# Optimization experiments

Measured on AMD Instinct MI355X. Metric: run time of the kernel, lower is better.

## Reference

```python
import jax, jax.numpy as jnp
import numpy as np

N_NODES = 50000
N_EDGES = 800000
IN_DIM = 64
HID = 64
NUM_GRAPHS = 512


def _gcn_conv(x, W, b, row, col, norm, n):
    # PyG GCNConv: h = x @ W; out[col] += norm * h[row]; out += b
    h = x @ W  # [N, HID]
    msg = h[row] * norm[:, None]  # [E', HID]
    out = jax.ops.segment_sum(msg, col, num_segments=n)
    return out + b


def setup_inputs() -> dict:
    key = jax.random.key(0)
    ks = jax.random.split(key, 12)
    x = jax.random.normal(ks[0], (N_NODES, IN_DIM), dtype=jnp.float32)
    edge_index = jax.random.randint(ks[1], (2, N_EDGES), 0, N_NODES, dtype=jnp.int64)
    batch = jnp.sort(jax.random.randint(ks[2], (N_NODES,), 0, NUM_GRAPHS, dtype=jnp.int64))
    s = 0.05
    W1 = jax.random.normal(ks[3], (IN_DIM, HID), dtype=jnp.float32) * s
    b1 = jnp.zeros((HID,), dtype=jnp.float32)
    W2 = jax.random.normal(ks[4], (HID, HID), dtype=jnp.float32) * s
    b2 = jnp.zeros((HID,), dtype=jnp.float32)
    W3 = jax.random.normal(ks[5], (HID, HID), dtype=jnp.float32) * s
    b3 = jnp.zeros((HID,), dtype=jnp.float32)
    lin_W = jax.random.normal(ks[6], (HID, 1), dtype=jnp.float32) * s
    lin_b = jnp.zeros((1,), dtype=jnp.float32)
    return {"x": x, "W1": W1, "b1": b1, "W2": W2, "b2": b2, "W3": W3,
            "b3": b3, "lin_W": lin_W, "lin_b": lin_b,
            "edge_index": edge_index, "batch": batch}


def reference(x, W1, b1, W2, b2, W3, b3, lin_W, lin_b, edge_index, batch):
    n = x.shape[0]
    # add self-loops (GCNConv default add_self_loops=True)
    loop = jnp.arange(n, dtype=edge_index.dtype)
    row = jnp.concatenate([edge_index[0], loop])  # source
    col = jnp.concatenate([edge_index[1], loop])  # target (aggregation index)
    # symmetric degree normalization: deg over targets with unit weights
    deg = jax.ops.segment_sum(jnp.ones_like(col, dtype=x.dtype), col, num_segments=n)
    dinv = jnp.where(deg > 0, jax.lax.rsqrt(deg), 0.0)
    norm = dinv[row] * dinv[col]  # [E+N]

    h = jax.nn.relu(_gcn_conv(x, W1, b1, row, col, norm, n))
    h = jax.nn.relu(_gcn_conv(h, W2, b2, row, col, norm, n))
    h = _gcn_conv(h, W3, b3, row, col, norm, n)

    # global_mean_pool over batch ids
    sums = jax.ops.segment_sum(h, batch, num_segments=NUM_GRAPHS)
    cnt = jax.ops.segment_sum(jnp.ones((n,), dtype=h.dtype), batch, num_segments=NUM_GRAPHS)
    pooled = sums / jnp.maximum(cnt, 1.0)[:, None]
    # dropout p=0.5 is identity in eval mode
    return pooled @ lin_W + lin_b  # [NUM_GRAPHS, 1]
```

## Files before the change

### kernel.cpp

```cpp
#include <hip/hip_runtime.h>
#include <hip/hip_fp16.h>

#define NN 50000
#define NE 800000
#define HD 64
#define NG 512
#define NBK 196
#define NBL 196
#define M_CNT (NBK * NBL)
#define NBS 151
#define GEMM_BLOCKS 3125


__global__ __launch_bounds__(256) void bucket_count(const int* __restrict__ col,
                                                    const int* __restrict__ batch,
                                                    int* __restrict__ counts,
                                                    int* __restrict__ beg,
                                                    int* __restrict__ endx,
                                                    float* __restrict__ pooled) {
    __shared__ int hist[256];
    int tid = threadIdx.x, blk = blockIdx.x;
    hist[tid] = 0;
    __syncthreads();
    int base = blk * 4096;
#pragma unroll
    for (int k = 0; k < 16; ++k) {
        int e = base + k * 256 + tid;
        if (e < NE) atomicAdd(&hist[col[e] >> 8], 1);
    }
    int t = blk * 256 + tid;
    if (t < NG * HD) pooled[t] = 0.f;
    if (t < NN) {
        int g = batch[t];
        if (t == 0 || batch[t - 1] != g) beg[g] = t;
        if (t == NN - 1 || batch[t + 1] != g) endx[g] = t + 1;
    }
    __syncthreads();
    if (tid < NBK) counts[tid * NBL + blk] = hist[tid];
}

__global__ __launch_bounds__(256) void block_reduce(const int* __restrict__ src,
                                                    int* __restrict__ bsum) {
    __shared__ int ws[4];
    int tid = threadIdx.x, lane = tid & 63, wid = tid >> 6;
    int i = blockIdx.x * 256 + tid;
    int v = (i < M_CNT) ? src[i] : 0;
#pragma unroll
    for (int off = 32; off > 0; off >>= 1) v += __shfl_down(v, off, 64);
    if (lane == 0) ws[wid] = v;
    __syncthreads();
    if (tid == 0) bsum[blockIdx.x] = ws[0] + ws[1] + ws[2] + ws[3];
}

__global__ __launch_bounds__(256) void block_scan(const int* __restrict__ src,
                                                  const int* __restrict__ bsum,
                                                  int* __restrict__ dst) {
    __shared__ int ws[4];
    __shared__ int spref;
    int tid = threadIdx.x, lane = tid & 63, wid = tid >> 6;
    int i = blockIdx.x * 256 + tid;
    int v = (i < M_CNT) ? src[i] : 0;
    int inc = v;
#pragma unroll
    for (int off = 1; off < 64; off <<= 1) {
        int t = __shfl_up(inc, off, 64);
        if (lane >= off) inc += t;
    }
    if (lane == 63) ws[wid] = inc;
    if (wid == 0) {
        int pref = 0;
        for (int base = 0; base < NBS; base += 64) {
            int k = base + lane;
            int bv = (k < NBS && k < blockIdx.x) ? bsum[k] : 0;
#pragma unroll
            for (int off = 32; off > 0; off >>= 1) bv += __shfl_down(bv, off, 64);
            pref += bv;
        }
        if (lane == 0) spref = pref;
    }
    __syncthreads();
    int woff = 0;
    for (int k = 0; k < wid; ++k) woff += ws[k];
    if (i < M_CNT) dst[i] = spref + woff + inc - v;
}

__global__ __launch_bounds__(256) void gemm1_scatter(const float* __restrict__ x,
                                                     const float* __restrict__ W1,
                                                     __half* __restrict__ h16,
                                                     const int* __restrict__ row,
                                                     const int* __restrict__ col,
                                                     const int* __restrict__ counts_ex,
                                                     unsigned* __restrict__ packed) {
    if (blockIdx.x < GEMM_BLOCKS) {
        __shared__ float Is[16][64];
        int t = threadIdx.x;
        int c = t & 63, r4 = t >> 6;
        float wcol[64];
#pragma unroll
        for (int k = 0; k < 64; ++k) wcol[k] = W1[k * HD + c];
        int row0 = blockIdx.x * 16;
        for (int i = t; i < 16 * 64; i += 256)
            Is[i >> 6][i & 63] = x[(row0 + (i >> 6)) * HD + (i & 63)];
        __syncthreads();
        float a0 = 0.f, a1 = 0.f, a2 = 0.f, a3 = 0.f;
        const float4* i0p = (const float4*)&Is[r4 + 0][0];
        const float4* i1p = (const float4*)&Is[r4 + 4][0];
        const float4* i2p = (const float4*)&Is[r4 + 8][0];
        const float4* i3p = (const float4*)&Is[r4 + 12][0];
#pragma unroll
        for (int q = 0; q < 16; ++q) {
            float4 i0 = i0p[q], i1 = i1p[q], i2 = i2p[q], i3 = i3p[q];
            float w0 = wcol[4 * q + 0], w1 = wcol[4 * q + 1];
            float w2 = wcol[4 * q + 2], w3 = wcol[4 * q + 3];
            a0 += i0.x * w0; a0 += i0.y * w1; a0 += i0.z * w2; a0 += i0.w * w3;
            a1 += i1.x * w0; a1 += i1.y * w1; a1 += i1.z * w2; a1 += i1.w * w3;
            a2 += i2.x * w0; a2 += i2.y * w1; a2 += i2.z * w2; a2 += i2.w * w3;
            a3 += i3.x * w0; a3 += i3.y * w1; a3 += i3.z * w2; a3 += i3.w * w3;
        }
        h16[(row0 + r4 + 0) * HD + c] = __float2half(a0);
        h16[(row0 + r4 + 4) * HD + c] = __float2half(a1);
        h16[(row0 + r4 + 8) * HD + c] = __float2half(a2);
        h16[(row0 + r4 + 12) * HD + c] = __float2half(a3);
    } else {
        __shared__ int cur[256];
        int tid = threadIdx.x, blk = blockIdx.x - GEMM_BLOCKS;
        cur[tid] = 0;
        __syncthreads();
        int base = blk * 4096;
#pragma unroll
        for (int k = 0; k < 16; ++k) {
            int e = base + k * 256 + tid;
            if (e < NE) {
                int c = col[e], r = row[e];
                int b = c >> 8;
                int lpos = atomicAdd(&cur[b], 1);
                int pos = counts_ex[b * NBL + blk] + lpos;
                packed[pos] = (unsigned)r | ((unsigned)(c & 255) << 16);
            }
        }
    }
}

__global__ __launch_bounds__(256) void csr_build(const unsigned* __restrict__ packed,
                                                 const int* __restrict__ counts_ex,
                                                 int* __restrict__ rowptr,
                                                 float* __restrict__ dinv,
                                                 __half* __restrict__ h16,
                                                 int* __restrict__ esrc) {
    __shared__ int hist[256];
    __shared__ int ws[4];
    __shared__ int lrp[256];
    __shared__ float sdinv[256];
    int bkt = blockIdx.x, tid = threadIdx.x;
    int s = counts_ex[bkt * NBL];
    int e = (bkt == NBK - 1) ? NE : counts_ex[(bkt + 1) * NBL];
    hist[tid] = 0;
    __syncthreads();
    for (int j = s + tid; j < e; j += 256)
        atomicAdd(&hist[(packed[j] >> 16) & 255], 1);
    __syncthreads();
    int lane = tid & 63, wid = tid >> 6;
    int v = hist[tid], inc = v;
#pragma unroll
    for (int off = 1; off < 64; off <<= 1) {
        int t = __shfl_up(inc, off, 64);
        if (lane >= off) inc += t;
    }
    if (lane == 63) ws[wid] = inc;
    __syncthreads();
    int woff = 0;
    for (int k = 0; k < wid; ++k) woff += ws[k];
    int excl = s + woff + inc - v;
    int node = bkt * 256 + tid;
    float dv = rsqrtf((float)(v + 1));
    if (node < NN) {
        rowptr[node] = excl;
        dinv[node] = dv;
    }
    if (bkt == 0 && tid == 0) rowptr[NN] = NE;
    lrp[tid] = excl;
    sdinv[tid] = dv;
    hist[tid] = 0;
    __syncthreads();
    {
        int nrows = (bkt == NBK - 1) ? (NN - 195 * 256) : 256;
        __half2* hb16 = (__half2*)(h16 + (size_t)bkt * 256 * HD);
        for (int i = tid; i < nrows * 32; i += 256) {
            float d = sdinv[i >> 5];
            float2 f = __half22float2(hb16[i]);
            hb16[i] = __floats2half2_rn(d * f.x, d * f.y);
        }
    }
    for (int j = s + tid; j < e; j += 256) {
        unsigned p = packed[j];
        int lc = (p >> 16) & 255;
        int slot = lrp[lc] + atomicAdd(&hist[lc], 1);
        esrc[slot] = (int)(p & 0xFFFF);
    }
}

template <bool POOL>
__global__ __launch_bounds__(256) void gather_fx(const __half* __restrict__ hp,
                                                 const int* __restrict__ rowptr,
                                                 const int* __restrict__ esrc,
                                                 const float* __restrict__ dinv,
                                                 const float* __restrict__ b,
                                                 const float* __restrict__ Wnext,
                                                 __half* __restrict__ hnext,
                                                 const int* __restrict__ batch,
                                                 float* __restrict__ pooled) {
    __shared__ float rowbuf[4][64];
    int tid = threadIdx.x, lane = tid & 63, wid = tid >> 6;
    int p = lane >> 5, c = lane & 31;
    int node = __builtin_amdgcn_readfirstlane(blockIdx.x * 4 + wid);
    const __half2* hv = (const __half2*)hp;

    float di = dinv[node];
    float2 self = __half22float2(hv[node * 32 + c]);
    float2 bb = ((const float2*)b)[c];

    float wcol[POOL ? 1 : 64];
    if (!POOL) {
#pragma unroll
        for (int k = 0; k < 64; ++k) wcol[k] = Wnext[k * HD + lane];
    }

    int s = rowptr[node], e = rowptr[node + 1];
    float2 acc = {0.f, 0.f};
    int j = s;
    for (; j + 8 <= e; j += 8) {
        int t0 = esrc[j + 0], t1 = esrc[j + 1], t2 = esrc[j + 2], t3 = esrc[j + 3];
        int t4 = esrc[j + 4], t5 = esrc[j + 5], t6 = esrc[j + 6], t7 = esrc[j + 7];
        int a0 = p ? t1 : t0;
        int a1 = p ? t3 : t2;
        int a2 = p ? t5 : t4;
        int a3 = p ? t7 : t6;
        float2 f0 = __half22float2(hv[a0 * 32 + c]);
        float2 f1 = __half22float2(hv[a1 * 32 + c]);
        float2 f2 = __half22float2(hv[a2 * 32 + c]);
        float2 f3 = __half22float2(hv[a3 * 32 + c]);
        acc.x += (f0.x + f1.x) + (f2.x + f3.x);
        acc.y += (f0.y + f1.y) + (f2.y + f3.y);
    }
    if (j < e) {
        int t0 = esrc[j + 0] & 0xFFFF, t1 = esrc[j + 1] & 0xFFFF;
        int t2 = esrc[j + 2] & 0xFFFF, t3 = esrc[j + 3] & 0xFFFF;
        int t4 = esrc[j + 4] & 0xFFFF, t5 = esrc[j + 5] & 0xFFFF;
        int t6 = esrc[j + 6] & 0xFFFF, t7 = esrc[j + 7] & 0xFFFF;
        int i0 = j + p, i1 = j + 2 + p, i2 = j + 4 + p, i3 = j + 6 + p;
        int a0 = p ? t1 : t0;
        int a1 = p ? t3 : t2;
        int a2 = p ? t5 : t4;
        int a3 = p ? t7 : t6;
        a0 = (i0 < e) ? a0 : t0;
        a1 = (i1 < e) ? a1 : t0;
        a2 = (i2 < e) ? a2 : t0;
        a3 = (i3 < e) ? a3 : t0;
        float m0 = (i0 < e) ? 1.f : 0.f;
        float m1 = (i1 < e) ? 1.f : 0.f;
        float m2 = (i2 < e) ? 1.f : 0.f;
        float m3 = (i3 < e) ? 1.f : 0.f;
        float2 f0 = __half22float2(hv[a0 * 32 + c]);
        float2 f1 = __half22float2(hv[a1 * 32 + c]);
        float2 f2 = __half22float2(hv[a2 * 32 + c]);
        float2 f3 = __half22float2(hv[a3 * 32 + c]);
        acc.x += m0 * f0.x + m1 * f1.x + m2 * f2.x + m3 * f3.x;
        acc.y += m0 * f0.y + m1 * f1.y + m2 * f2.y + m3 * f3.y;
    }
    acc.x += __shfl_xor(acc.x, 32, 64);
    acc.y += __shfl_xor(acc.y, 32, 64);

    if (POOL) {
        if (p == 0) {
            float vx = di * (acc.x + self.x) + bb.x;
            float vy = di * (acc.y + self.y) + bb.y;
            int g = batch[node];
            atomicAdd(&pooled[g * HD + 2 * c], vx);
            atomicAdd(&pooled[g * HD + 2 * c + 1], vy);
        }
    } else {
        if (p == 0) {
            rowbuf[wid][2 * c]     = fmaxf(di * (acc.x + self.x) + bb.x, 0.f);
            rowbuf[wid][2 * c + 1] = fmaxf(di * (acc.y + self.y) + bb.y, 0.f);
        }
        float outc = 0.f;
        const float4* rb4 = (const float4*)&rowbuf[wid][0];
#pragma unroll
        for (int jj = 0; jj < 16; ++jj) {
            float4 r = rb4[jj];
            outc += r.x * wcol[4 * jj + 0] + r.y * wcol[4 * jj + 1]
                  + r.z * wcol[4 * jj + 2] + r.w * wcol[4 * jj + 3];
        }
        hnext[(size_t)node * HD + lane] = __float2half(di * outc);
    }
}

__global__ __launch_bounds__(64) void final_kernel(const float* __restrict__ pooled,
                                                   const int* __restrict__ beg,
                                                   const int* __restrict__ endx,
                                                   const float* __restrict__ lin_W,
                                                   const float* __restrict__ lin_b,
                                                   float* __restrict__ out) {
    int g = blockIdx.x, d = threadIdx.x;
    float cnt = (float)(endx[g] - beg[g]);
    float v = pooled[g * HD + d] / fmaxf(cnt, 1.f) * lin_W[d];
#pragma unroll
    for (int off = 32; off > 0; off >>= 1) v += __shfl_down(v, off, 64);
    if (d == 0) out[g] = v + lin_b[0];
}

extern "C" void kernel_launch(void* const* d_in, const int* in_sizes, int n_in,
                              void* d_out, int out_size, void* d_ws, size_t ws_size,
                              hipStream_t stream) {
    const float* x     = (const float*)d_in[0];
    const float* W1    = (const float*)d_in[1];
    const float* b1    = (const float*)d_in[2];
    const float* W2    = (const float*)d_in[3];
    const float* b2    = (const float*)d_in[4];
    const float* W3    = (const float*)d_in[5];
    const float* b3    = (const float*)d_in[6];
    const float* lin_W = (const float*)d_in[7];
    const float* lin_b = (const float*)d_in[8];
    const int* edge_index = (const int*)d_in[9];
    const int* batch      = (const int*)d_in[10];
    const int* row = edge_index;
    const int* col = edge_index + NE;
    float* out = (float*)d_out;

    __half*   h16a      = (__half*)d_ws;
    __half*   h16b      = h16a + (size_t)NN * HD;
    int*      esrc      = (int*)(h16b + (size_t)NN * HD);
    unsigned* packed    = (unsigned*)(esrc + NE + 64);
    int*      counts    = (int*)(packed + NE);
    int*      counts_ex = counts + M_CNT;
    int*      rowptr    = counts_ex + M_CNT;
    float*    dinv      = (float*)(rowptr + NN + 2);
    int*      bsum      = (int*)(dinv + NN);
    float*    pooled    = (float*)(bsum + 256);
    int*      beg       = (int*)(pooled + NG * HD);
    int*      endx      = beg + NG;

    bucket_count<<<NBL, 256, 0, stream>>>(col, batch, counts, beg, endx, pooled);
    block_reduce<<<NBS, 256, 0, stream>>>(counts, bsum);
    block_scan<<<NBS, 256, 0, stream>>>(counts, bsum, counts_ex);
    gemm1_scatter<<<GEMM_BLOCKS + NBL, 256, 0, stream>>>(x, W1, h16a, row, col,
                                                         counts_ex, packed);
    csr_build<<<NBK, 256, 0, stream>>>(packed, counts_ex, rowptr, dinv,
                                       h16a, esrc);

    const int GB = NN / 4;

    gather_fx<false><<<GB, 256, 0, stream>>>(h16a, rowptr, esrc, dinv, b1, W2,
                                             h16b, batch, pooled);
    gather_fx<false><<<GB, 256, 0, stream>>>(h16b, rowptr, esrc, dinv, b2, W3,
                                             h16a, batch, pooled);
    gather_fx<true><<<GB, 256, 0, stream>>>(h16a, rowptr, esrc, dinv, b3, nullptr,
                                            nullptr, batch, pooled);

    final_kernel<<<NG, 64, 0, stream>>>(pooled, beg, endx, lin_W, lin_b, out);
}
```

Before: 255.3 us.

## Replace two-level bucket CSR build with per-node atomic counting and scatter

Drops the bucketed counting sort (bucket counts, reduce and scan, packed scatter, per-bucket CSR build) in favour of per-node global atomic degree counts, a single scan over nodes that also writes dinv, and a direct atomic-cursor scatter of source ids into esrc. The dinv scaling moves into the first GEMM epilogue, so there is no separate pass that rescales h16. Launch count falls from five kernels to a memset plus three. In exchange, each edge now does a global atomic on a random node counter, both at count time and at fill time. Edge order within a row also becomes nondeterministic, which changes the fp16 summation order.

Result: slower. 296.7 us (+16.2%).

```diff
diff --git a/kernel.cpp b/kernel.cpp
--- a/kernel.cpp
+++ b/kernel.cpp
@@ -7,26 +7,29 @@
 #define NG 512
 #define NBK 196
 #define NBL 196
-#define M_CNT (NBK * NBL)
-#define NBS 151
 #define GEMM_BLOCKS 3125
 
 
-__global__ __launch_bounds__(256) void bucket_count(const int* __restrict__ col,
-                                                    const int* __restrict__ batch,
-                                                    int* __restrict__ counts,
-                                                    int* __restrict__ beg,
-                                                    int* __restrict__ endx,
-                                                    float* __restrict__ pooled) {
-    __shared__ int hist[256];
+__global__ __launch_bounds__(256) void hist(const int* __restrict__ col,
+                                            const int* __restrict__ batch,
+                                            int* __restrict__ cnt,
+                                            int* __restrict__ bsum,
+                                            int* __restrict__ beg,
+                                            int* __restrict__ endx,
+                                            float* __restrict__ pooled) {
+    __shared__ int histL[256];
     int tid = threadIdx.x, blk = blockIdx.x;
-    hist[tid] = 0;
+    histL[tid] = 0;
     __syncthreads();
     int base = blk * 4096;
 #pragma unroll
     for (int k = 0; k < 16; ++k) {
         int e = base + k * 256 + tid;
-        if (e < NE) atomicAdd(&hist[col[e] >> 8], 1);
+        if (e < NE) {
+            int c = col[e];
+            atomicAdd(&cnt[c], 1);
+            atomicAdd(&histL[c >> 8], 1);
+        }
     }
     int t = blk * 256 + tid;
     if (t < NG * HD) pooled[t] = 0.f;
@@ -36,30 +39,19 @@
         if (t == NN - 1 || batch[t + 1] != g) endx[g] = t + 1;
     }
     __syncthreads();
-    if (tid < NBK) counts[tid * NBL + blk] = hist[tid];
-}
-
-__global__ __launch_bounds__(256) void block_reduce(const int* __restrict__ src,
-                                                    int* __restrict__ bsum) {
-    __shared__ int ws[4];
-    int tid = threadIdx.x, lane = tid & 63, wid = tid >> 6;
-    int i = blockIdx.x * 256 + tid;
-    int v = (i < M_CNT) ? src[i] : 0;
-#pragma unroll
-    for (int off = 32; off > 0; off >>= 1) v += __shfl_down(v, off, 64);
-    if (lane == 0) ws[wid] = v;
-    __syncthreads();
-    if (tid == 0) bsum[blockIdx.x] = ws[0] + ws[1] + ws[2] + ws[3];
-}
-
-__global__ __launch_bounds__(256) void block_scan(const int* __restrict__ src,
-                                                  const int* __restrict__ bsum,
-                                                  int* __restrict__ dst) {
+    if (tid < NBK) atomicAdd(&bsum[tid], histL[tid]);
+}
+
+__global__ __launch_bounds__(256) void nscan(const int* __restrict__ cnt,
+                                             const int* __restrict__ bsum,
+                                             int* __restrict__ rowptr,
+                                             int* __restrict__ cursor,
+                                             float* __restrict__ dinv) {
     __shared__ int ws[4];
     __shared__ int spref;
     int tid = threadIdx.x, lane = tid & 63, wid = tid >> 6;
     int i = blockIdx.x * 256 + tid;
-    int v = (i < M_CNT) ? src[i] : 0;
+    int v = (i < NN) ? cnt[i] : 0;
     int inc = v;
 #pragma unroll
     for (int off = 1; off < 64; off <<= 1) {
@@ -69,9 +61,9 @@
     if (lane == 63) ws[wid] = inc;
     if (wid == 0) {
         int pref = 0;
-        for (int base = 0; base < NBS; base += 64) {
+        for (int base = 0; base < NBK; base += 64) {
             int k = base + lane;
-            int bv = (k < NBS && k < blockIdx.x) ? bsum[k] : 0;
+            int bv = (k < NBK && k < blockIdx.x) ? bsum[k] : 0;
 #pragma unroll
             for (int off = 32; off > 0; off >>= 1) bv += __shfl_down(bv, off, 64);
             pref += bv;
@@ -81,16 +73,23 @@
     __syncthreads();
     int woff = 0;
     for (int k = 0; k < wid; ++k) woff += ws[k];
-    if (i < M_CNT) dst[i] = spref + woff + inc - v;
-}
-
-__global__ __launch_bounds__(256) void gemm1_scatter(const float* __restrict__ x,
-                                                     const float* __restrict__ W1,
-                                                     __half* __restrict__ h16,
-                                                     const int* __restrict__ row,
-                                                     const int* __restrict__ col,
-                                                     const int* __restrict__ counts_ex,
-                                                     unsigned* __restrict__ packed) {
+    if (i < NN) {
+        int excl = spref + woff + inc - v;
+        rowptr[i] = excl;
+        cursor[i] = excl;
+        dinv[i] = rsqrtf((float)(v + 1));
+    }
+    if (i == 0) rowptr[NN] = NE;
+}
+
+__global__ __launch_bounds__(256) void gemm1_fill(const float* __restrict__ x,
+                                                  const float* __restrict__ W1,
+                                                  const float* __restrict__ dinv,
+                                                  __half* __restrict__ h16,
+                                                  const int* __restrict__ row,
+                                                  const int* __restrict__ col,
+                                                  int* __restrict__ cursor,
+                                                  int* __restrict__ esrc) {
     if (blockIdx.x < GEMM_BLOCKS) {
         __shared__ float Is[16][64];
         int t = threadIdx.x;
@@ -99,6 +98,10 @@
 #pragma unroll
         for (int k = 0; k < 64; ++k) wcol[k] = W1[k * HD + c];
         int row0 = blockIdx.x * 16;
+        float d0 = dinv[row0 + r4 + 0];
+        float d1 = dinv[row0 + r4 + 4];
+        float d2 = dinv[row0 + r4 + 8];
+        float d3 = dinv[row0 + r4 + 12];
         for (int i = t; i < 16 * 64; i += 256)
             Is[i >> 6][i & 63] = x[(row0 + (i >> 6)) * HD + (i & 63)];
         __syncthreads();
@@ -117,85 +120,22 @@
             a2 += i2.x * w0; a2 += i2.y * w1; a2 += i2.z * w2; a2 += i2.w * w3;
             a3 += i3.x * w0; a3 += i3.y * w1; a3 += i3.z * w2; a3 += i3.w * w3;
         }
-        h16[(row0 + r4 + 0) * HD + c] = __float2half(a0);
-        h16[(row0 + r4 + 4) * HD + c] = __float2half(a1);
-        h16[(row0 + r4 + 8) * HD + c] = __float2half(a2);
-        h16[(row0 + r4 + 12) * HD + c] = __float2half(a3);
+        h16[(row0 + r4 + 0) * HD + c] = __float2half(d0 * a0);
+        h16[(row0 + r4 + 4) * HD + c] = __float2half(d1 * a1);
+        h16[(row0 + r4 + 8) * HD + c] = __float2half(d2 * a2);
+        h16[(row0 + r4 + 12) * HD + c] = __float2half(d3 * a3);
     } else {
-        __shared__ int cur[256];
         int tid = threadIdx.x, blk = blockIdx.x - GEMM_BLOCKS;
-        cur[tid] = 0;
-        __syncthreads();
         int base = blk * 4096;
 #pragma unroll
         for (int k = 0; k < 16; ++k) {
             int e = base + k * 256 + tid;
             if (e < NE) {
-                int c = col[e], r = row[e];
-                int b = c >> 8;
-                int lpos = atomicAdd(&cur[b], 1);
-                int pos = counts_ex[b * NBL + blk] + lpos;
-                packed[pos] = (unsigned)r | ((unsigned)(c & 255) << 16);
+                int c = col[e];
+                int pos = atomicAdd(&cursor[c], 1);
+                esrc[pos] = row[e];
             }
         }
-    }
-}
-
-__global__ __launch_bounds__(256) void csr_build(const unsigned* __restrict__ packed,
-                                                 const int* __restrict__ counts_ex,
-                                                 int* __restrict__ rowptr,
-                                                 float* __restrict__ dinv,
-                                                 __half* __restrict__ h16,
-                                                 int* __restrict__ esrc) {
-    __shared__ int hist[256];
-    __shared__ int ws[4];
-    __shared__ int lrp[256];
-    __shared__ float sdinv[256];
-    int bkt = blockIdx.x, tid = threadIdx.x;
-    int s = counts_ex[bkt * NBL];
-    int e = (bkt == NBK - 1) ? NE : counts_ex[(bkt + 1) * NBL];
-    hist[tid] = 0;
-    __syncthreads();
-    for (int j = s + tid; j < e; j += 256)
-        atomicAdd(&hist[(packed[j] >> 16) & 255], 1);
-    __syncthreads();
-    int lane = tid & 63, wid = tid >> 6;
-    int v = hist[tid], inc = v;
-#pragma unroll
-    for (int off = 1; off < 64; off <<= 1) {
-        int t = __shfl_up(inc, off, 64);
-        if (lane >= off) inc += t;
-    }
-    if (lane == 63) ws[wid] = inc;
-    __syncthreads();
-    int woff = 0;
-    for (int k = 0; k < wid; ++k) woff += ws[k];
-    int excl = s + woff + inc - v;
-    int node = bkt * 256 + tid;
-    float dv = rsqrtf((float)(v + 1));
-    if (node < NN) {
-        rowptr[node] = excl;
-        dinv[node] = dv;
-    }
-    if (bkt == 0 && tid == 0) rowptr[NN] = NE;
-    lrp[tid] = excl;
-    sdinv[tid] = dv;
-    hist[tid] = 0;
-    __syncthreads();
-    {
-        int nrows = (bkt == NBK - 1) ? (NN - 195 * 256) : 256;
-        __half2* hb16 = (__half2*)(h16 + (size_t)bkt * 256 * HD);
-        for (int i = tid; i < nrows * 32; i += 256) {
-            float d = sdinv[i >> 5];
-            float2 f = __half22float2(hb16[i]);
-            hb16[i] = __floats2half2_rn(d * f.x, d * f.y);
-        }
-    }
-    for (int j = s + tid; j < e; j += 256) {
-        unsigned p = packed[j];
-        int lc = (p >> 16) & 255;
-        int slot = lrp[lc] + atomicAdd(&hist[lc], 1);
-        esrc[slot] = (int)(p & 0xFFFF);
     }
 }
 
@@ -330,23 +270,20 @@
     __half*   h16a      = (__half*)d_ws;
     __half*   h16b      = h16a + (size_t)NN * HD;
     int*      esrc      = (int*)(h16b + (size_t)NN * HD);
-    unsigned* packed    = (unsigned*)(esrc + NE + 64);
-    int*      counts    = (int*)(packed + NE);
-    int*      counts_ex = counts + M_CNT;
-    int*      rowptr    = counts_ex + M_CNT;
+    int*      cnt       = esrc + NE + 64;
+    int*      bsum      = cnt + NN;
+    int*      cursor    = bsum + 256;
+    int*      rowptr    = cursor + NN;
     float*    dinv      = (float*)(rowptr + NN + 2);
-    int*      bsum      = (int*)(dinv + NN);
-    float*    pooled    = (float*)(bsum + 256);
+    float*    pooled    = (float*)(dinv + NN);
     int*      beg       = (int*)(pooled + NG * HD);
     int*      endx      = beg + NG;
 
-    bucket_count<<<NBL, 256, 0, stream>>>(col, batch, counts, beg, endx, pooled);
-    block_reduce<<<NBS, 256, 0, stream>>>(counts, bsum);
-    block_scan<<<NBS, 256, 0, stream>>>(counts, bsum, counts_ex);
-    gemm1_scatter<<<GEMM_BLOCKS + NBL, 256, 0, stream>>>(x, W1, h16a, row, col,
-                                                         counts_ex, packed);
-    csr_build<<<NBK, 256, 0, stream>>>(packed, counts_ex, rowptr, dinv,
-                                       h16a, esrc);
+    hipMemsetAsync(cnt, 0, (size_t)(NN + 256) * sizeof(int), stream);
+    hist<<<NBL, 256, 0, stream>>>(col, batch, cnt, bsum, beg, endx, pooled);
+    nscan<<<NBK, 256, 0, stream>>>(cnt, bsum, rowptr, cursor, dinv);
+    gemm1_fill<<<GEMM_BLOCKS + NBL, 256, 0, stream>>>(x, W1, dinv, h16a, row,
+                                                      col, cursor, esrc);
 
     const int GB = NN / 4;
 
```

## Compute per-node degree with global atomics and fold dinv scaling into GEMM1

Applied to the files above, without the earlier changes.

Counts in-degrees per node with global atomics during bucket counting, a new pass over all 800k targets. The first GEMM's output is scaled by dinv directly, which removes the separate read-modify-write of h16 in csr_build. The rowptr scan moves into extra blocks of the gemm/scatter launch. The leaner csr_fill kernel now only places edge sources, and the gather kernels recompute dinv from the counts. The trade is global atomic contention plus a memset, in exchange for dropping a histogram pass and an h16 rescale pass.

After: 275.9 us. +8.1%, slower.

```diff
diff --git a/kernel.cpp b/kernel.cpp
--- a/kernel.cpp
+++ b/kernel.cpp
@@ -14,6 +14,7 @@
 
 __global__ __launch_bounds__(256) void bucket_count(const int* __restrict__ col,
                                                     const int* __restrict__ batch,
+                                                    int* __restrict__ cnt,
                                                     int* __restrict__ counts,
                                                     int* __restrict__ beg,
                                                     int* __restrict__ endx,
@@ -26,7 +27,11 @@
 #pragma unroll
     for (int k = 0; k < 16; ++k) {
         int e = base + k * 256 + tid;
-        if (e < NE) atomicAdd(&hist[col[e] >> 8], 1);
+        if (e < NE) {
+            int c = col[e];
+            atomicAdd(&cnt[c], 1);
+            atomicAdd(&hist[c >> 8], 1);
+        }
     }
     int t = blk * 256 + tid;
     if (t < NG * HD) pooled[t] = 0.f;
@@ -86,11 +91,13 @@
 
 __global__ __launch_bounds__(256) void gemm1_scatter(const float* __restrict__ x,
                                                      const float* __restrict__ W1,
+                                                     const int* __restrict__ cnt,
                                                      __half* __restrict__ h16,
                                                      const int* __restrict__ row,
                                                      const int* __restrict__ col,
                                                      const int* __restrict__ counts_ex,
-                                                     unsigned* __restrict__ packed) {
+                                                     unsigned* __restrict__ packed,
+                                                     int* __restrict__ rowptr) {
     if (blockIdx.x < GEMM_BLOCKS) {
         __shared__ float Is[16][64];
         int t = threadIdx.x;
@@ -99,6 +106,10 @@
 #pragma unroll
         for (int k = 0; k < 64; ++k) wcol[k] = W1[k * HD + c];
         int row0 = blockIdx.x * 16;
+        float d0 = rsqrtf((float)(cnt[row0 + r4 + 0] + 1));
+        float d1 = rsqrtf((float)(cnt[row0 + r4 + 4] + 1));
+        float d2 = rsqrtf((float)(cnt[row0 + r4 + 8] + 1));
+        float d3 = rsqrtf((float)(cnt[row0 + r4 + 12] + 1));
         for (int i = t; i < 16 * 64; i += 256)
             Is[i >> 6][i & 63] = x[(row0 + (i >> 6)) * HD + (i & 63)];
         __syncthreads();
@@ -117,11 +128,11 @@
             a2 += i2.x * w0; a2 += i2.y * w1; a2 += i2.z * w2; a2 += i2.w * w3;
             a3 += i3.x * w0; a3 += i3.y * w1; a3 += i3.z * w2; a3 += i3.w * w3;
         }
-        h16[(row0 + r4 + 0) * HD + c] = __float2half(a0);
-        h16[(row0 + r4 + 4) * HD + c] = __float2half(a1);
-        h16[(row0 + r4 + 8) * HD + c] = __float2half(a2);
-        h16[(row0 + r4 + 12) * HD + c] = __float2half(a3);
-    } else {
+        h16[(row0 + r4 + 0) * HD + c] = __float2half(d0 * a0);
+        h16[(row0 + r4 + 4) * HD + c] = __float2half(d1 * a1);
+        h16[(row0 + r4 + 8) * HD + c] = __float2half(d2 * a2);
+        h16[(row0 + r4 + 12) * HD + c] = __float2half(d3 * a3);
+    } else if (blockIdx.x < GEMM_BLOCKS + NBL) {
         __shared__ int cur[256];
         int tid = threadIdx.x, blk = blockIdx.x - GEMM_BLOCKS;
         cur[tid] = 0;
@@ -138,63 +149,44 @@
                 packed[pos] = (unsigned)r | ((unsigned)(c & 255) << 16);
             }
         }
-    }
-}
-
-__global__ __launch_bounds__(256) void csr_build(const unsigned* __restrict__ packed,
-                                                 const int* __restrict__ counts_ex,
-                                                 int* __restrict__ rowptr,
-                                                 float* __restrict__ dinv,
-                                                 __half* __restrict__ h16,
-                                                 int* __restrict__ esrc) {
-    __shared__ int hist[256];
-    __shared__ int ws[4];
+    } else {
+        __shared__ int ws[4];
+        int b = blockIdx.x - (GEMM_BLOCKS + NBL);
+        int tid = threadIdx.x, lane = tid & 63, wid = tid >> 6;
+        int node = b * 256 + tid;
+        int v = (node < NN) ? cnt[node] : 0;
+        int inc = v;
+#pragma unroll
+        for (int off = 1; off < 64; off <<= 1) {
+            int t = __shfl_up(inc, off, 64);
+            if (lane >= off) inc += t;
+        }
+        if (lane == 63) ws[wid] = inc;
+        __syncthreads();
+        int woff = 0;
+        for (int k = 0; k < wid; ++k) woff += ws[k];
+        int s0 = counts_ex[b * NBL];
+        if (node <= NN) rowptr[node] = s0 + woff + inc - v;
+    }
+}
+
+__global__ __launch_bounds__(256) void csr_fill(const unsigned* __restrict__ packed,
+                                                const int* __restrict__ counts_ex,
+                                                const int* __restrict__ rowptr,
+                                                int* __restrict__ esrc) {
     __shared__ int lrp[256];
-    __shared__ float sdinv[256];
+    __shared__ int cur[256];
     int bkt = blockIdx.x, tid = threadIdx.x;
     int s = counts_ex[bkt * NBL];
     int e = (bkt == NBK - 1) ? NE : counts_ex[(bkt + 1) * NBL];
-    hist[tid] = 0;
-    __syncthreads();
-    for (int j = s + tid; j < e; j += 256)
-        atomicAdd(&hist[(packed[j] >> 16) & 255], 1);
-    __syncthreads();
-    int lane = tid & 63, wid = tid >> 6;
-    int v = hist[tid], inc = v;
-#pragma unroll
-    for (int off = 1; off < 64; off <<= 1) {
-        int t = __shfl_up(inc, off, 64);
-        if (lane >= off) inc += t;
-    }
-    if (lane == 63) ws[wid] = inc;
-    __syncthreads();
-    int woff = 0;
-    for (int k = 0; k < wid; ++k) woff += ws[k];
-    int excl = s + woff + inc - v;
     int node = bkt * 256 + tid;
-    float dv = rsqrtf((float)(v + 1));
-    if (node < NN) {
-        rowptr[node] = excl;
-        dinv[node] = dv;
-    }
-    if (bkt == 0 && tid == 0) rowptr[NN] = NE;
-    lrp[tid] = excl;
-    sdinv[tid] = dv;
-    hist[tid] = 0;
-    __syncthreads();
-    {
-        int nrows = (bkt == NBK - 1) ? (NN - 195 * 256) : 256;
-        __half2* hb16 = (__half2*)(h16 + (size_t)bkt * 256 * HD);
-        for (int i = tid; i < nrows * 32; i += 256) {
-            float d = sdinv[i >> 5];
-            float2 f = __half22float2(hb16[i]);
-            hb16[i] = __floats2half2_rn(d * f.x, d * f.y);
-        }
-    }
+    lrp[tid] = (node < NN) ? rowptr[node] : 0;
+    cur[tid] = 0;
+    __syncthreads();
     for (int j = s + tid; j < e; j += 256) {
         unsigned p = packed[j];
         int lc = (p >> 16) & 255;
-        int slot = lrp[lc] + atomicAdd(&hist[lc], 1);
+        int slot = lrp[lc] + atomicAdd(&cur[lc], 1);
         esrc[slot] = (int)(p & 0xFFFF);
     }
 }
@@ -203,7 +195,7 @@
 __global__ __launch_bounds__(256) void gather_fx(const __half* __restrict__ hp,
                                                  const int* __restrict__ rowptr,
                                                  const int* __restrict__ esrc,
-                                                 const float* __restrict__ dinv,
+                                                 const int* __restrict__ cnt,
                                                  const float* __restrict__ b,
                                                  const float* __restrict__ Wnext,
                                                  __half* __restrict__ hnext,
@@ -215,7 +207,7 @@
     int node = __builtin_amdgcn_readfirstlane(blockIdx.x * 4 + wid);
     const __half2* hv = (const __half2*)hp;
 
-    float di = dinv[node];
+    float di = rsqrtf((float)(cnt[node] + 1));
     float2 self = __half22float2(hv[node * 32 + c]);
     float2 bb = ((const float2*)b)[c];
 
@@ -333,28 +325,29 @@
     unsigned* packed    = (unsigned*)(esrc + NE + 64);
     int*      counts    = (int*)(packed + NE);
     int*      counts_ex = counts + M_CNT;
-    int*      rowptr    = counts_ex + M_CNT;
-    float*    dinv      = (float*)(rowptr + NN + 2);
-    int*      bsum      = (int*)(dinv + NN);
+    int*      cnt       = counts_ex + M_CNT;
+    int*      rowptr    = cnt + NN;
+    int*      bsum      = rowptr + NN + 2;
     float*    pooled    = (float*)(bsum + 256);
     int*      beg       = (int*)(pooled + NG * HD);
     int*      endx      = beg + NG;
 
-    bucket_count<<<NBL, 256, 0, stream>>>(col, batch, counts, beg, endx, pooled);
+    hipMemsetAsync(cnt, 0, (size_t)NN * sizeof(int), stream);
+    bucket_count<<<NBL, 256, 0, stream>>>(col, batch, cnt, counts, beg, endx,
+                                          pooled);
     block_reduce<<<NBS, 256, 0, stream>>>(counts, bsum);
     block_scan<<<NBS, 256, 0, stream>>>(counts, bsum, counts_ex);
-    gemm1_scatter<<<GEMM_BLOCKS + NBL, 256, 0, stream>>>(x, W1, h16a, row, col,
-                                                         counts_ex, packed);
-    csr_build<<<NBK, 256, 0, stream>>>(packed, counts_ex, rowptr, dinv,
-                                       h16a, esrc);
+    gemm1_scatter<<<GEMM_BLOCKS + NBL + NBK, 256, 0, stream>>>(
+        x, W1, cnt, h16a, row, col, counts_ex, packed, rowptr);
+    csr_fill<<<NBK, 256, 0, stream>>>(packed, counts_ex, rowptr, esrc);
 
     const int GB = NN / 4;
 
-    gather_fx<false><<<GB, 256, 0, stream>>>(h16a, rowptr, esrc, dinv, b1, W2,
+    gather_fx<false><<<GB, 256, 0, stream>>>(h16a, rowptr, esrc, cnt, b1, W2,
                                              h16b, batch, pooled);
-    gather_fx<false><<<GB, 256, 0, stream>>>(h16b, rowptr, esrc, dinv, b2, W3,
+    gather_fx<false><<<GB, 256, 0, stream>>>(h16b, rowptr, esrc, cnt, b2, W3,
                                              h16a, batch, pooled);
-    gather_fx<true><<<GB, 256, 0, stream>>>(h16a, rowptr, esrc, dinv, b3, nullptr,
+    gather_fx<true><<<GB, 256, 0, stream>>>(h16a, rowptr, esrc, cnt, b3, nullptr,
                                             nullptr, batch, pooled);
 
     final_kernel<<<NG, 64, 0, stream>>>(pooled, beg, endx, lin_W, lin_b, out);
```

## Fold bucket prefix-scan kernels into scatter and CSR-build kernels

Applied to the files above, without the earlier changes.

Removes the separate block_reduce and block_scan launches. Each scatter block now recomputes its bucket base offsets by summing rows of the count matrix and doing an in-block scan, and csr_build recomputes the bucket start offsets the same way. This saves two kernel launches and the counts_ex round trip through memory. In exchange, every scatter and CSR block re-reads the full 196x196 count matrix with strided per-thread loops, which is redundant work.

Result: slower. 266.3 us (+4.3%).

```diff
diff --git a/kernel.cpp b/kernel.cpp
--- a/kernel.cpp
+++ b/kernel.cpp
@@ -8,7 +8,6 @@
 #define NBK 196
 #define NBL 196
 #define M_CNT (NBK * NBL)
-#define NBS 151
 #define GEMM_BLOCKS 3125
 
 
@@ -39,57 +38,12 @@
     if (tid < NBK) counts[tid * NBL + blk] = hist[tid];
 }
 
-__global__ __launch_bounds__(256) void block_reduce(const int* __restrict__ src,
-                                                    int* __restrict__ bsum) {
-    __shared__ int ws[4];
-    int tid = threadIdx.x, lane = tid & 63, wid = tid >> 6;
-    int i = blockIdx.x * 256 + tid;
-    int v = (i < M_CNT) ? src[i] : 0;
-#pragma unroll
-    for (int off = 32; off > 0; off >>= 1) v += __shfl_down(v, off, 64);
-    if (lane == 0) ws[wid] = v;
-    __syncthreads();
-    if (tid == 0) bsum[blockIdx.x] = ws[0] + ws[1] + ws[2] + ws[3];
-}
-
-__global__ __launch_bounds__(256) void block_scan(const int* __restrict__ src,
-                                                  const int* __restrict__ bsum,
-                                                  int* __restrict__ dst) {
-    __shared__ int ws[4];
-    __shared__ int spref;
-    int tid = threadIdx.x, lane = tid & 63, wid = tid >> 6;
-    int i = blockIdx.x * 256 + tid;
-    int v = (i < M_CNT) ? src[i] : 0;
-    int inc = v;
-#pragma unroll
-    for (int off = 1; off < 64; off <<= 1) {
-        int t = __shfl_up(inc, off, 64);
-        if (lane >= off) inc += t;
-    }
-    if (lane == 63) ws[wid] = inc;
-    if (wid == 0) {
-        int pref = 0;
-        for (int base = 0; base < NBS; base += 64) {
-            int k = base + lane;
-            int bv = (k < NBS && k < blockIdx.x) ? bsum[k] : 0;
-#pragma unroll
-            for (int off = 32; off > 0; off >>= 1) bv += __shfl_down(bv, off, 64);
-            pref += bv;
-        }
-        if (lane == 0) spref = pref;
-    }
-    __syncthreads();
-    int woff = 0;
-    for (int k = 0; k < wid; ++k) woff += ws[k];
-    if (i < M_CNT) dst[i] = spref + woff + inc - v;
-}
-
 __global__ __launch_bounds__(256) void gemm1_scatter(const float* __restrict__ x,
                                                      const float* __restrict__ W1,
                                                      __half* __restrict__ h16,
                                                      const int* __restrict__ row,
                                                      const int* __restrict__ col,
-                                                     const int* __restrict__ counts_ex,
+                                                     const int* __restrict__ counts,
                                                      unsigned* __restrict__ packed) {
     if (blockIdx.x < GEMM_BLOCKS) {
         __shared__ float Is[16][64];
@@ -122,8 +76,32 @@
         h16[(row0 + r4 + 8) * HD + c] = __float2half(a2);
         h16[(row0 + r4 + 12) * HD + c] = __float2half(a3);
     } else {
+        __shared__ int ws[4];
+        __shared__ int bas[256];
         __shared__ int cur[256];
         int tid = threadIdx.x, blk = blockIdx.x - GEMM_BLOCKS;
+        int lane = tid & 63, wid = tid >> 6;
+        int colpart = 0, rowsum = 0;
+        if (tid < NBK) {
+            const int* rowp = counts + tid * NBL;
+#pragma unroll 4
+            for (int k = 0; k < NBL; ++k) {
+                int v = rowp[k];
+                rowsum += v;
+                colpart += (k < blk) ? v : 0;
+            }
+        }
+        int inc = rowsum;
+#pragma unroll
+        for (int off = 1; off < 64; off <<= 1) {
+            int tt = __shfl_up(inc, off, 64);
+            if (lane >= off) inc += tt;
+        }
+        if (lane == 63) ws[wid] = inc;
+        __syncthreads();
+        int woff = 0;
+        for (int k = 0; k < wid; ++k) woff += ws[k];
+        bas[tid] = (woff + inc - rowsum) + colpart;
         cur[tid] = 0;
         __syncthreads();
         int base = blk * 4096;
@@ -134,15 +112,14 @@
                 int c = col[e], r = row[e];
                 int b = c >> 8;
                 int lpos = atomicAdd(&cur[b], 1);
-                int pos = counts_ex[b * NBL + blk] + lpos;
-                packed[pos] = (unsigned)r | ((unsigned)(c & 255) << 16);
+                packed[bas[b] + lpos] = (unsigned)r | ((unsigned)(c & 255) << 16);
             }
         }
     }
 }
 
 __global__ __launch_bounds__(256) void csr_build(const unsigned* __restrict__ packed,
-                                                 const int* __restrict__ counts_ex,
+                                                 const int* __restrict__ counts,
                                                  int* __restrict__ rowptr,
                                                  float* __restrict__ dinv,
                                                  __half* __restrict__ h16,
@@ -151,15 +128,35 @@
     __shared__ int ws[4];
     __shared__ int lrp[256];
     __shared__ float sdinv[256];
+    __shared__ int sstart[257];
     int bkt = blockIdx.x, tid = threadIdx.x;
-    int s = counts_ex[bkt * NBL];
-    int e = (bkt == NBK - 1) ? NE : counts_ex[(bkt + 1) * NBL];
+    int lane = tid & 63, wid = tid >> 6;
+    {
+        int rowsum = 0;
+        if (tid < NBK) {
+            const int* rowp = counts + tid * NBL;
+#pragma unroll 4
+            for (int k = 0; k < NBL; ++k) rowsum += rowp[k];
+        }
+        int inc = rowsum;
+#pragma unroll
+        for (int off = 1; off < 64; off <<= 1) {
+            int tt = __shfl_up(inc, off, 64);
+            if (lane >= off) inc += tt;
+        }
+        if (lane == 63) ws[wid] = inc;
+        __syncthreads();
+        int woff = 0;
+        for (int k = 0; k < wid; ++k) woff += ws[k];
+        sstart[tid] = woff + inc - rowsum;
+        if (tid == 255) sstart[256] = woff + inc;
+    }
     hist[tid] = 0;
     __syncthreads();
+    int s = sstart[bkt], e = sstart[bkt + 1];
     for (int j = s + tid; j < e; j += 256)
         atomicAdd(&hist[(packed[j] >> 16) & 255], 1);
     __syncthreads();
-    int lane = tid & 63, wid = tid >> 6;
     int v = hist[tid], inc = v;
 #pragma unroll
     for (int off = 1; off < 64; off <<= 1) {
@@ -332,20 +329,16 @@
     int*      esrc      = (int*)(h16b + (size_t)NN * HD);
     unsigned* packed    = (unsigned*)(esrc + NE + 64);
     int*      counts    = (int*)(packed + NE);
-    int*      counts_ex = counts + M_CNT;
-    int*      rowptr    = counts_ex + M_CNT;
+    int*      rowptr    = counts + M_CNT;
     float*    dinv      = (float*)(rowptr + NN + 2);
-    int*      bsum      = (int*)(dinv + NN);
-    float*    pooled    = (float*)(bsum + 256);
+    float*    pooled    = (float*)(dinv + NN);
     int*      beg       = (int*)(pooled + NG * HD);
     int*      endx      = beg + NG;
 
     bucket_count<<<NBL, 256, 0, stream>>>(col, batch, counts, beg, endx, pooled);
-    block_reduce<<<NBS, 256, 0, stream>>>(counts, bsum);
-    block_scan<<<NBS, 256, 0, stream>>>(counts, bsum, counts_ex);
     gemm1_scatter<<<GEMM_BLOCKS + NBL, 256, 0, stream>>>(x, W1, h16a, row, col,
-                                                         counts_ex, packed);
-    csr_build<<<NBK, 256, 0, stream>>>(packed, counts_ex, rowptr, dinv,
+                                                         counts, packed);
+    csr_build<<<NBK, 256, 0, stream>>>(packed, counts, rowptr, dinv,
                                        h16a, esrc);
 
     const int GB = NN / 4;
```
